# Optimization experiments

Measured on AMD Instinct MI355X. Metric: run time of the kernel, lower is better.

## Reference

```python
import jax, jax.numpy as jnp
import numpy as np


def setup_inputs() -> dict:
    key = jax.random.key(0)
    k1, k2 = jax.random.split(key)
    Nd, Ld, E = 128, 128, 128   # docs, doc sentences, embed_size
    Nq, Lq = 128, 32            # queries, query sentences
    # ColBERT-style: embeddings are L2-normalized per sentence in embed()
    doc = jax.random.normal(k1, (Nd, Ld, E), dtype=jnp.float32)
    doc = doc / jnp.linalg.norm(doc, axis=-1, keepdims=True)
    # query embeddings are stored transposed: [Nq, E, Lq]
    q = jax.random.normal(k2, (Nq, Lq, E), dtype=jnp.float32)
    q = q / jnp.linalg.norm(q, axis=-1, keepdims=True)
    query = jnp.transpose(q, (0, 2, 1))  # [Nq, E, Lq]
    return {"doc_tokens": doc, "query_tokens": query}


def reference(doc_tokens, query_tokens):
    # max_sim(doc, query, sentence_wise=False, full_mat=True)
    # doc_tokens: [Nd, Ld, E]; query_tokens: [Nq, E, Lq]
    # scores[q,d,t,l] = sum_e doc[d,t,e] * query[q,e,l]   (bmm over cross product)
    scores = jnp.einsum('dte,qel->qdtl', doc_tokens, query_tokens)
    # max over doc tokens t, sum over query tokens l -> [Nq, Nd]
    return jnp.sum(jnp.max(scores, axis=2), axis=-1)
```

## Files before the change

### kernel.cpp

```cpp
#include <hip/hip_runtime.h>
#include <hip/hip_bf16.h>

typedef short short8 __attribute__((ext_vector_type(8)));
typedef float f32x4  __attribute__((ext_vector_type(4)));

#define ND 128
#define LD 128
#define EE 128
#define NQ 128
#define LQ 32
#define LDS_STRIDE 136
#define GDOCS 2

__global__ __launch_bounds__(256)
void convert_kernel(const float* __restrict__ doc, const float* __restrict__ qry,
                    __hip_bfloat16* __restrict__ docB, __hip_bfloat16* __restrict__ qB) {
  const int tid = threadIdx.x;
  if (blockIdx.x < 2048) {
    int gid = blockIdx.x * 256 + tid;
    float4 v = reinterpret_cast<const float4*>(doc)[gid];
    union { ushort4 u; __hip_bfloat16 b[4]; } o;
    o.b[0] = __float2bfloat16(v.x);
    o.b[1] = __float2bfloat16(v.y);
    o.b[2] = __float2bfloat16(v.z);
    o.b[3] = __float2bfloat16(v.w);
    reinterpret_cast<ushort4*>(docB)[gid] = o.u;
    return;
  }
  __shared__ float s[LQ][EE + 1];
  const int q = blockIdx.x - 2048;
  const float* src = qry + q * (EE * LQ);
  #pragma unroll
  for (int i = 0; i < 4; ++i) {
    int c = i * 256 + tid;
    int e = c >> 3;
    int l = (c & 7) << 2;
    float4 v = reinterpret_cast<const float4*>(src)[c];
    s[l + 0][e] = v.x;
    s[l + 1][e] = v.y;
    s[l + 2][e] = v.z;
    s[l + 3][e] = v.w;
  }
  __syncthreads();
  __hip_bfloat16* dst = qB + q * (LQ * EE);
  #pragma unroll
  for (int i = 0; i < 4; ++i) {
    int c = i * 256 + tid;
    int l = c >> 5;
    int e = (c & 31) << 2;
    union { ushort4 u; __hip_bfloat16 b[4]; } o;
    o.b[0] = __float2bfloat16(s[l][e + 0]);
    o.b[1] = __float2bfloat16(s[l][e + 1]);
    o.b[2] = __float2bfloat16(s[l][e + 2]);
    o.b[3] = __float2bfloat16(s[l][e + 3]);
    reinterpret_cast<ushort4*>(dst)[c] = o.u;
  }
}

__global__ __launch_bounds__(256)
void maxsim_kernel(const __hip_bfloat16* __restrict__ docB,
                   const __hip_bfloat16* __restrict__ qB,
                   float* __restrict__ out) {
  __shared__ __hip_bfloat16 sdoc[LD * LDS_STRIDE];
  const int d0   = blockIdx.x * GDOCS;
  const int qblk = blockIdx.y;
  const int tid  = threadIdx.x;
  const int wave = tid >> 6;
  const int lane = tid & 63;
  const int ln15 = lane & 15;
  const int quad = lane >> 4;
  const int q0   = qblk * 8 + wave * 2;

  short8 bfrag[2][2][4];
  #pragma unroll
  for (int qq = 0; qq < 2; ++qq) {
    const __hip_bfloat16* qp = qB + (q0 + qq) * (LQ * EE);
    #pragma unroll
    for (int nt = 0; nt < 2; ++nt)
      #pragma unroll
      for (int ks = 0; ks < 4; ++ks)
        bfrag[qq][nt][ks] = *reinterpret_cast<const short8*>(
            qp + (nt * 16 + ln15) * EE + ks * 32 + quad * 8);
  }

  #pragma unroll 1
  for (int g = 0; g < GDOCS; ++g) {
    const int d = d0 + g;
    __syncthreads();
    {
      const uint4* src = reinterpret_cast<const uint4*>(docB + d * (LD * EE));
      #pragma unroll
      for (int it = 0; it < 8; ++it) {
        int idx = it * 256 + tid;
        int row = idx >> 4;
        int c8  = (idx & 15) << 3;
        *reinterpret_cast<uint4*>(&sdoc[row * LDS_STRIDE + c8]) =  src[idx];
      }
    }
    __syncthreads();

    float colmax[2][2] = {{-3.0e38f, -3.0e38f}, {-3.0e38f, -3.0e38f}};

    #pragma unroll
    for (int mt = 0; mt < 8; ++mt) {
      f32x4 acc[2][2];
      #pragma unroll
      for (int qq = 0; qq < 2; ++qq)
        #pragma unroll
        for (int nt = 0; nt < 2; ++nt)
          acc[qq][nt] = (f32x4){0.f, 0.f, 0.f, 0.f};

      #pragma unroll
      for (int ks = 0; ks < 4; ++ks) {
        short8 a = *reinterpret_cast<const short8*>(
            &sdoc[(mt * 16 + ln15) * LDS_STRIDE + ks * 32 + quad * 8]);
        acc[0][0] = __builtin_amdgcn_mfma_f32_16x16x32_bf16(a, bfrag[0][0][ks], acc[0][0], 0, 0, 0);
        acc[0][1] = __builtin_amdgcn_mfma_f32_16x16x32_bf16(a, bfrag[0][1][ks], acc[0][1], 0, 0, 0);
        acc[1][0] = __builtin_amdgcn_mfma_f32_16x16x32_bf16(a, bfrag[1][0][ks], acc[1][0], 0, 0, 0);
        acc[1][1] = __builtin_amdgcn_mfma_f32_16x16x32_bf16(a, bfrag[1][1][ks], acc[1][1], 0, 0, 0);
      }

      #pragma unroll
      for (int qq = 0; qq < 2; ++qq)
        #pragma unroll
        for (int nt = 0; nt < 2; ++nt)
          colmax[qq][nt] = fmaxf(colmax[qq][nt],
                                 fmaxf(fmaxf(acc[qq][nt][0], acc[qq][nt][1]),
                                       fmaxf(acc[qq][nt][2], acc[qq][nt][3])));
    }

    #pragma unroll
    for (int qq = 0; qq < 2; ++qq) {
      float m0 = colmax[qq][0];
      float m1 = colmax[qq][1];
      m0 = fmaxf(m0, __shfl_xor(m0, 16, 64));
      m0 = fmaxf(m0, __shfl_xor(m0, 32, 64));
      m1 = fmaxf(m1, __shfl_xor(m1, 16, 64));
      m1 = fmaxf(m1, __shfl_xor(m1, 32, 64));
      float s = m0 + m1;
      s += __shfl_xor(s, 1, 64);
      s += __shfl_xor(s, 2, 64);
      s += __shfl_xor(s, 4, 64);
      s += __shfl_xor(s, 8, 64);
      if (lane == 0) out[(q0 + qq) * ND + d] = s;
    }
  }
}

extern "C" void kernel_launch(void* const* d_in, const int* in_sizes, int n_in,
                              void* d_out, int out_size, void* d_ws, size_t ws_size,
                              hipStream_t stream) {
  const float* doc = (const float*)d_in[0];
  const float* qry = (const float*)d_in[1];
  float* out = (float*)d_out;

  __hip_bfloat16* docB = (__hip_bfloat16*)d_ws;
  __hip_bfloat16* qB   = docB + ND * LD * EE;

  convert_kernel<<<dim3(2048 + NQ), dim3(256), 0, stream>>>(doc, qry, docB, qB);
  maxsim_kernel<<<dim3(ND / GDOCS, NQ / 8), dim3(256), 0, stream>>>(docB, qB, out);
}
```

Baseline: 82.49 us.

## Double-buffer doc tiles in LDS with register prefetch and 512-thread blocks

The maxsim kernel now uses 512 threads (8 waves), so each block covers 16 queries instead of 8 and the grid shrinks by half. The second doc's tile is loaded into registers while the first doc is being computed, then written to a second LDS buffer. This hides global-load latency and cuts per-block doc reloads. LDS use doubles to about 68KB per block, which may lower occupancy, and the grid drops to 512 blocks.

```diff
diff --git a/kernel.cpp b/kernel.cpp
--- a/kernel.cpp
+++ b/kernel.cpp
@@ -10,7 +10,7 @@
 #define NQ 128
 #define LQ 32
 #define LDS_STRIDE 136
-#define GDOCS 2
+#define LDSH (LD * LDS_STRIDE)
 
 __global__ __launch_bounds__(256)
 void convert_kernel(const float* __restrict__ doc, const float* __restrict__ qry,
@@ -57,19 +57,19 @@
   }
 }
 
-__global__ __launch_bounds__(256)
+__global__ __launch_bounds__(512)
 void maxsim_kernel(const __hip_bfloat16* __restrict__ docB,
                    const __hip_bfloat16* __restrict__ qB,
                    float* __restrict__ out) {
-  __shared__ __hip_bfloat16 sdoc[LD * LDS_STRIDE];
-  const int d0   = blockIdx.x * GDOCS;
+  __shared__ __hip_bfloat16 sdoc[2][LDSH];
+  const int d0   = blockIdx.x * 2;
   const int qblk = blockIdx.y;
   const int tid  = threadIdx.x;
   const int wave = tid >> 6;
   const int lane = tid & 63;
   const int ln15 = lane & 15;
   const int quad = lane >> 4;
-  const int q0   = qblk * 8 + wave * 2;
+  const int q0   = qblk * 16 + wave * 2;
 
   short8 bfrag[2][2][4];
   #pragma unroll
@@ -83,21 +83,27 @@
             qp + (nt * 16 + ln15) * EE + ks * 32 + quad * 8);
   }
 
+  uint4 pf[4];
+  {
+    const uint4* src = reinterpret_cast<const uint4*>(docB + d0 * (LD * EE));
+    #pragma unroll
+    for (int it = 0; it < 4; ++it) pf[it] = src[it * 512 + tid];
+    #pragma unroll
+    for (int it = 0; it < 4; ++it) {
+      int idx = it * 512 + tid;
+      *reinterpret_cast<uint4*>(
+          &sdoc[0][(idx >> 4) * LDS_STRIDE + ((idx & 15) << 3)]) = pf[it];
+    }
+  }
+  __syncthreads();
+
   #pragma unroll 1
-  for (int g = 0; g < GDOCS; ++g) {
-    const int d = d0 + g;
-    __syncthreads();
-    {
-      const uint4* src = reinterpret_cast<const uint4*>(docB + d * (LD * EE));
+  for (int g = 0; g < 2; ++g) {
+    if (g == 0) {
+      const uint4* src = reinterpret_cast<const uint4*>(docB + (d0 + 1) * (LD * EE));
       #pragma unroll
-      for (int it = 0; it < 8; ++it) {
-        int idx = it * 256 + tid;
-        int row = idx >> 4;
-        int c8  = (idx & 15) << 3;
-        *reinterpret_cast<uint4*>(&sdoc[row * LDS_STRIDE + c8]) =  src[idx];
-      }
+      for (int it = 0; it < 4; ++it) pf[it] = src[it * 512 + tid];
     }
-    __syncthreads();
 
     float colmax[2][2] = {{-3.0e38f, -3.0e38f}, {-3.0e38f, -3.0e38f}};
 
@@ -113,7 +119,7 @@
       #pragma unroll
       for (int ks = 0; ks < 4; ++ks) {
         short8 a = *reinterpret_cast<const short8*>(
-            &sdoc[(mt * 16 + ln15) * LDS_STRIDE + ks * 32 + quad * 8]);
+            &sdoc[g][(mt * 16 + ln15) * LDS_STRIDE + ks * 32 + quad * 8]);
         acc[0][0] = __builtin_amdgcn_mfma_f32_16x16x32_bf16(a, bfrag[0][0][ks], acc[0][0], 0, 0, 0);
         acc[0][1] = __builtin_amdgcn_mfma_f32_16x16x32_bf16(a, bfrag[0][1][ks], acc[0][1], 0, 0, 0);
         acc[1][0] = __builtin_amdgcn_mfma_f32_16x16x32_bf16(a, bfrag[1][0][ks], acc[1][0], 0, 0, 0);
@@ -129,6 +135,15 @@
                                        fmaxf(acc[qq][nt][2], acc[qq][nt][3])));
     }
 
+    if (g == 0) {
+      #pragma unroll
+      for (int it = 0; it < 4; ++it) {
+        int idx = it * 512 + tid;
+        *reinterpret_cast<uint4*>(
+            &sdoc[1][(idx >> 4) * LDS_STRIDE + ((idx & 15) << 3)]) = pf[it];
+      }
+    }
+
     #pragma unroll
     for (int qq = 0; qq < 2; ++qq) {
       float m0 = colmax[qq][0];
@@ -142,8 +157,10 @@
       s += __shfl_xor(s, 2, 64);
       s += __shfl_xor(s, 4, 64);
       s += __shfl_xor(s, 8, 64);
-      if (lane == 0) out[(q0 + qq) * ND + d] = s;
+      if (lane == 0) out[(q0 + qq) * ND + d0 + g] = s;
     }
+
+    if (g == 0) __syncthreads();
   }
 }
 
@@ -158,5 +175,5 @@
   __hip_bfloat16* qB   = docB + ND * LD * EE;
 
   convert_kernel<<<dim3(2048 + NQ), dim3(256), 0, stream>>>(doc, qry, docB, qB);
-  maxsim_kernel<<<dim3(ND / GDOCS, NQ / 8), dim3(256), 0, stream>>>(docB, qB, out);
+  maxsim_kernel<<<dim3(ND / 2, NQ / 16), dim3(512), 0, stream>>>(docB, qB, out);
 }
```

After: 87.25 us. 1.06x slower.
